# Performance work log

Measured on AMD Instinct MI355X. Metric: run time of the kernel, lower is better.

The kernel has to match this reference:

```python
import jax, jax.numpy as jnp
import numpy as np

ANGLE = 0.5  # angular margin from init_kwargs


def setup_inputs() -> dict:
    key = jax.random.key(0)
    k1, k2, k3 = jax.random.split(key, 3)
    B, F, C = 512, 128, 100000
    # scale by 0.1 so exp(features @ w) and exp(modulus * cos) stay finite in fp32
    features = jax.random.normal(k1, (B, F), dtype=jnp.float32) * 0.1
    w = jax.random.normal(k2, (F, C), dtype=jnp.float32) * 0.1
    target = jax.random.randint(k3, (B,), 0, C, dtype=jnp.int64)
    return {"features": features, "w": w, "target": target}


def reference(features, w, target):
    B = features.shape[0]
    rows = jnp.arange(B)
    # norms: [B,1] and [1,C]
    features_modulus = jnp.sqrt(jnp.sum(features ** 2, axis=1, keepdims=True))
    w_modulus = jnp.sqrt(jnp.sum(w ** 2, axis=0, keepdims=True))
    modulus = features_modulus * w_modulus  # [B, C]
    logits = jnp.matmul(features, w)  # [B, C] (computed once; torch computes it twice)
    cos_theta = logits / modulus / 1.01
    theta = jnp.arccos(cos_theta) + ANGLE
    cos_theta_plus = jnp.cos(theta)
    margin_logits = modulus * cos_theta_plus  # [B, C]
    top = jnp.exp(margin_logits[rows, target])  # [B]
    down_ = jnp.exp(logits)  # [B, C]
    down = jnp.sum(down_, axis=1) - down_[rows, target] + top  # [B]
    return -jnp.sum(jnp.log(top / down)) / B
```

## Files before the change

### kernel.cpp

```cpp
#include <hip/hip_runtime.h>

#define F_DIM 128
#define C_DIM 100000
#define B_ROWS 512
#define ANGLE 0.5f
#define CPB 128
#define NCB 782
#define OOB_PAD 96.0f

typedef __attribute__((ext_vector_type(4))) float  f32x4;
typedef __attribute__((ext_vector_type(8))) short  bf16x8;

static __device__ __forceinline__ short f2bf(float x) {
    unsigned int u = __float_as_uint(x);
    u += 0x7FFFu + ((u >> 16) & 1u);
    return (short)(u >> 16);
}

__global__ __launch_bounds__(512, 4)
void arc_main(const float* __restrict__ feat,
              const float* __restrict__ w,
              float* __restrict__ pp)
{
    __shared__ unsigned short lBt[128 * 128];

    const int tid = threadIdx.x;
    const int cb  = blockIdx.x;
    const int c0  = cb * CPB;
    const int r0  = blockIdx.y * 256;

    const int lane = tid & 63;
    const int wv   = tid >> 6;
    const int quad = lane >> 4;
    const int l15  = lane & 15;

    bf16x8 fB[2][4];
    #pragma unroll
    for (int s = 0; s < 2; ++s) {
        const int b = r0 + wv * 32 + s * 16 + l15;
        #pragma unroll
        for (int ks = 0; ks < 4; ++ks) {
            const int k0 = ks * 32 + quad * 8;
            const f32x4 u0 = *(const f32x4*)(feat + b * F_DIM + k0);
            const f32x4 u1 = *(const f32x4*)(feat + b * F_DIM + k0 + 4);
            bf16x8 h;
            h[0] = f2bf(u0[0]); h[1] = f2bf(u0[1]); h[2] = f2bf(u0[2]); h[3] = f2bf(u0[3]);
            h[4] = f2bf(u1[0]); h[5] = f2bf(u1[1]); h[6] = f2bf(u1[2]); h[7] = f2bf(u1[3]);
            fB[s][ks] = h;
        }
    }

    {
        const int c  = tid & 127;
        const int g  = tid >> 7;
        const int gc = c0 + c;
        #pragma unroll
        for (int j = 0; j < 4; ++j) {
            float v[8];
            #pragma unroll
            for (int i = 0; i < 8; ++i) {
                const int k = g * 32 + j * 8 + i;
                v[i] = (gc < C_DIM) ? w[(size_t)k * C_DIM + gc] : 0.f;
            }
            bf16x8 h;
            #pragma unroll
            for (int i = 0; i < 8; ++i) h[i] = f2bf(v[i]);
            const int pc = (g * 4 + j) ^ (c & 15);
            *(bf16x8*)&lBt[c * 128 + pc * 8] = h;
        }
    }
    __syncthreads();

    float eA0 = 0.f, eA1 = 0.f, eA2 = 0.f, eA3 = 0.f;
    float eB0 = 0.f, eB1 = 0.f, eB2 = 0.f, eB3 = 0.f;
    #pragma unroll
    for (int m = 0; m < 8; ++m) {
        f32x4 a0 = {0.f, 0.f, 0.f, 0.f};
        f32x4 a1 = {0.f, 0.f, 0.f, 0.f};
        const int row = m * 16 + l15;
        #pragma unroll
        for (int ks = 0; ks < 4; ++ks) {
            const int pc = (ks * 4 + quad) ^ (row & 15);
            const bf16x8 af = *(const bf16x8*)&lBt[row * 128 + pc * 8];
            a0 = __builtin_amdgcn_mfma_f32_16x16x32_bf16(af, fB[0][ks], a0, 0, 0, 0);
            a1 = __builtin_amdgcn_mfma_f32_16x16x32_bf16(af, fB[1][ks], a1, 0, 0, 0);
        }
        eA0 += __expf(a0[0]); eA1 += __expf(a0[1]);
        eA2 += __expf(a0[2]); eA3 += __expf(a0[3]);
        eB0 += __expf(a1[0]); eB1 += __expf(a1[1]);
        eB2 += __expf(a1[2]); eB3 += __expf(a1[3]);
    }

    float esum0 = (eA0 + eA1) + (eA2 + eA3);
    float esum1 = (eB0 + eB1) + (eB2 + eB3);
    esum0 += __shfl_xor(esum0, 16); esum0 += __shfl_xor(esum0, 32);
    esum1 += __shfl_xor(esum1, 16); esum1 += __shfl_xor(esum1, 32);
    if (lane < 16) {
        pp[(size_t)cb * 512 + r0 + wv * 32 + lane]      = esum0;
        pp[(size_t)cb * 512 + r0 + wv * 32 + 16 + lane] = esum1;
    }
}

__global__ void arc_row(const float* __restrict__ feat,
                        const float* __restrict__ w,
                        const int*   __restrict__ target,
                        const float* __restrict__ pp,
                        float* __restrict__ term)
{
    const int b    = blockIdx.x;
    const int lane = threadIdx.x;
    const int t    = target[b];

    float dot = 0.f, wsq = 0.f, fsq = 0.f, rs = 0.f;
    #pragma unroll
    for (int h = 0; h < 2; ++h) {
        const int f  = lane + h * 64;
        const float fv = feat[b * F_DIM + f];
        const float wv = w[(size_t)f * C_DIM + t];
        dot += fv * wv;
        wsq += wv * wv;
        fsq += fv * fv;
    }
    for (int j = lane; j < NCB; j += 64)
        rs += pp[(size_t)j * 512 + b];

    #pragma unroll
    for (int off = 32; off > 0; off >>= 1) {
        dot += __shfl_xor(dot, off);
        wsq += __shfl_xor(wsq, off);
        fsq += __shfl_xor(fsq, off);
        rs  += __shfl_xor(rs,  off);
    }
    if (lane == 0) {
        const float mod = sqrtf(fsq) * sqrtf(wsq);
        float ct = dot / (mod * 1.01f);
        ct = fminf(1.f, fmaxf(-1.f, ct));
        const float th   = acosf(ct) + ANGLE;
        const float marg = mod * cosf(th);
        const float down = rs - OOB_PAD - expf(dot) + expf(marg);
        term[b] = marg - logf(down);
    }
}

__global__ void arc_loss(const float* __restrict__ term,
                         float* __restrict__ out)
{
    __shared__ float red[B_ROWS];
    const int b = threadIdx.x;
    red[b] = term[b];
    __syncthreads();
    #pragma unroll
    for (int st = 256; st > 0; st >>= 1) {
        if (b < st) red[b] += red[b + st];
        __syncthreads();
    }
    if (b == 0) out[0] = -red[0] / (float)B_ROWS;
}

extern "C" void kernel_launch(void* const* d_in, const int* in_sizes, int n_in,
                              void* d_out, int out_size, void* d_ws, size_t ws_size,
                              hipStream_t stream)
{
    const float* feat   = (const float*)d_in[0];
    const float* w      = (const float*)d_in[1];
    const int*   target = (const int*)d_in[2];

    float* pp   = (float*)d_ws;
    float* term = pp + (size_t)NCB * 512;

    arc_main<<<dim3(NCB, 2), 512, 0, stream>>>(feat, w, pp);
    arc_row<<<B_ROWS, 64, 0, stream>>>(feat, w, target, pp, term);
    arc_loss<<<1, B_ROWS, 0, stream>>>(term, (float*)d_out);
}
```

Measured before the change: 131.5 us.

## Vectorize weight tile load, use hardware bf16 packing and exp2, transpose partials

The weight tile is now loaded as float4 vectors (four classes per thread across eight feature rows) instead of scalar loads, with a new LDS swizzle to match. fp32-to-bf16 conversion uses the packed hardware instruction instead of manual rounding. log2(e) is folded into the weights so the epilogue can use the native exp2. The partial-sum buffer is transposed to row-major so the row kernel reads contiguous memory. These target the global load and VALU cost of staging and the exp work, at the cost of a more intricate swizzle and scaling before the bf16 rounding.

Result: faster. 128.8 us (-2.1%).

```diff
diff --git a/kernel.cpp b/kernel.cpp
--- a/kernel.cpp
+++ b/kernel.cpp
@@ -1,20 +1,22 @@
 #include <hip/hip_runtime.h>
 
-#define F_DIM 128
-#define C_DIM 100000
-#define B_ROWS 512
-#define ANGLE 0.5f
-#define CPB 128
-#define NCB 782
+#define F_DIM   128
+#define C_DIM   100000
+#define B_ROWS  512
+#define ANGLE   0.5f
+#define CPB     128
+#define NCB     782
 #define OOB_PAD 96.0f
+#define LOG2E   1.4426950408889634f
 
-typedef __attribute__((ext_vector_type(4))) float  f32x4;
-typedef __attribute__((ext_vector_type(8))) short  bf16x8;
+typedef __attribute__((ext_vector_type(4))) float        f32x4;
+typedef __attribute__((ext_vector_type(8))) short        bf16x8;
+typedef __attribute__((ext_vector_type(4))) unsigned int u32x4;
 
-static __device__ __forceinline__ short f2bf(float x) {
-    unsigned int u = __float_as_uint(x);
-    u += 0x7FFFu + ((u >> 16) & 1u);
-    return (short)(u >> 16);
+static __device__ __forceinline__ unsigned int pk2(float a, float b) {
+    unsigned int r;
+    asm("v_cvt_pk_bf16_f32 %0, %1, %2" : "=v"(r) : "v"(a), "v"(b));
+    return r;
 }
 
 __global__ __launch_bounds__(512, 4)
@@ -24,15 +26,42 @@
 {
     __shared__ unsigned short lBt[128 * 128];
 
-    const int tid = threadIdx.x;
-    const int cb  = blockIdx.x;
-    const int c0  = cb * CPB;
-    const int r0  = blockIdx.y * 256;
-
+    const int tid  = threadIdx.x;
+    const int cb   = blockIdx.x;
+    const int c0   = cb * CPB;
+    const int r0   = blockIdx.y * 256;
     const int lane = tid & 63;
     const int wv   = tid >> 6;
     const int quad = lane >> 4;
     const int l15  = lane & 15;
+
+    {
+        const int cq = tid & 31;
+        const int ko = tid >> 5;
+        const int gc = c0 + cq * 4;
+        f32x4 wr[8];
+        if (gc < C_DIM) {
+            const float* wp = w + (size_t)ko * 8 * C_DIM + gc;
+            #pragma unroll
+            for (int i = 0; i < 8; ++i)
+                wr[i] = *(const f32x4*)(wp + (size_t)i * C_DIM);
+        } else {
+            #pragma unroll
+            for (int i = 0; i < 8; ++i)
+                wr[i] = (f32x4){0.f, 0.f, 0.f, 0.f};
+        }
+        #pragma unroll
+        for (int j = 0; j < 4; ++j) {
+            const int cls = cq * 4 + j;
+            union { u32x4 u; bf16x8 h; } c;
+            c.u[0] = pk2(wr[0][j] * LOG2E, wr[1][j] * LOG2E);
+            c.u[1] = pk2(wr[2][j] * LOG2E, wr[3][j] * LOG2E);
+            c.u[2] = pk2(wr[4][j] * LOG2E, wr[5][j] * LOG2E);
+            c.u[3] = pk2(wr[6][j] * LOG2E, wr[7][j] * LOG2E);
+            const int f = (cls & 12) | ((cls ^ (cls >> 4)) & 3);
+            *(bf16x8*)&lBt[cls * 128 + ((ko ^ f) << 3)] = c.h;
+        }
+    }
 
     bf16x8 fB[2][4];
     #pragma unroll
@@ -43,30 +72,10 @@
             const int k0 = ks * 32 + quad * 8;
             const f32x4 u0 = *(const f32x4*)(feat + b * F_DIM + k0);
             const f32x4 u1 = *(const f32x4*)(feat + b * F_DIM + k0 + 4);
-            bf16x8 h;
-            h[0] = f2bf(u0[0]); h[1] = f2bf(u0[1]); h[2] = f2bf(u0[2]); h[3] = f2bf(u0[3]);
-            h[4] = f2bf(u1[0]); h[5] = f2bf(u1[1]); h[6] = f2bf(u1[2]); h[7] = f2bf(u1[3]);
-            fB[s][ks] = h;
-        }
-    }
-
-    {
-        const int c  = tid & 127;
-        const int g  = tid >> 7;
-        const int gc = c0 + c;
-        #pragma unroll
-        for (int j = 0; j < 4; ++j) {
-            float v[8];
-            #pragma unroll
-            for (int i = 0; i < 8; ++i) {
-                const int k = g * 32 + j * 8 + i;
-                v[i] = (gc < C_DIM) ? w[(size_t)k * C_DIM + gc] : 0.f;
-            }
-            bf16x8 h;
-            #pragma unroll
-            for (int i = 0; i < 8; ++i) h[i] = f2bf(v[i]);
-            const int pc = (g * 4 + j) ^ (c & 15);
-            *(bf16x8*)&lBt[c * 128 + pc * 8] = h;
+            union { u32x4 u; bf16x8 h; } c;
+            c.u[0] = pk2(u0[0], u0[1]); c.u[1] = pk2(u0[2], u0[3]);
+            c.u[2] = pk2(u1[0], u1[1]); c.u[3] = pk2(u1[2], u1[3]);
+            fB[s][ks] = c.h;
         }
     }
     __syncthreads();
@@ -77,18 +86,19 @@
     for (int m = 0; m < 8; ++m) {
         f32x4 a0 = {0.f, 0.f, 0.f, 0.f};
         f32x4 a1 = {0.f, 0.f, 0.f, 0.f};
-        const int row = m * 16 + l15;
+        const int rb = (m * 16 + l15) * 128;
+        const int fr = (l15 & 12) | ((l15 ^ m) & 3);
         #pragma unroll
         for (int ks = 0; ks < 4; ++ks) {
-            const int pc = (ks * 4 + quad) ^ (row & 15);
-            const bf16x8 af = *(const bf16x8*)&lBt[row * 128 + pc * 8];
+            const int pc = (ks * 4 + quad) ^ fr;
+            const bf16x8 af = *(const bf16x8*)&lBt[rb + (pc << 3)];
             a0 = __builtin_amdgcn_mfma_f32_16x16x32_bf16(af, fB[0][ks], a0, 0, 0, 0);
             a1 = __builtin_amdgcn_mfma_f32_16x16x32_bf16(af, fB[1][ks], a1, 0, 0, 0);
         }
-        eA0 += __expf(a0[0]); eA1 += __expf(a0[1]);
-        eA2 += __expf(a0[2]); eA3 += __expf(a0[3]);
-        eB0 += __expf(a1[0]); eB1 += __expf(a1[1]);
-        eB2 += __expf(a1[2]); eB3 += __expf(a1[3]);
+        eA0 += __builtin_amdgcn_exp2f(a0[0]); eA1 += __builtin_amdgcn_exp2f(a0[1]);
+        eA2 += __builtin_amdgcn_exp2f(a0[2]); eA3 += __builtin_amdgcn_exp2f(a0[3]);
+        eB0 += __builtin_amdgcn_exp2f(a1[0]); eB1 += __builtin_amdgcn_exp2f(a1[1]);
+        eB2 += __builtin_amdgcn_exp2f(a1[2]); eB3 += __builtin_amdgcn_exp2f(a1[3]);
     }
 
     float esum0 = (eA0 + eA1) + (eA2 + eA3);
@@ -96,8 +106,9 @@
     esum0 += __shfl_xor(esum0, 16); esum0 += __shfl_xor(esum0, 32);
     esum1 += __shfl_xor(esum1, 16); esum1 += __shfl_xor(esum1, 32);
     if (lane < 16) {
-        pp[(size_t)cb * 512 + r0 + wv * 32 + lane]      = esum0;
-        pp[(size_t)cb * 512 + r0 + wv * 32 + 16 + lane] = esum1;
+        const int r = r0 + wv * 32 + lane;
+        pp[(size_t)r * NCB + cb]        = esum0;
+        pp[(size_t)(r + 16) * NCB + cb] = esum1;
     }
 }
 
@@ -114,15 +125,18 @@
     float dot = 0.f, wsq = 0.f, fsq = 0.f, rs = 0.f;
     #pragma unroll
     for (int h = 0; h < 2; ++h) {
-        const int f  = lane + h * 64;
+        const int f   = lane + h * 64;
         const float fv = feat[b * F_DIM + f];
-        const float wv = w[(size_t)f * C_DIM + t];
-        dot += fv * wv;
-        wsq += wv * wv;
+        const float wc = w[(size_t)f * C_DIM + t];
+        dot += fv * wc;
+        wsq += wc * wc;
         fsq += fv * fv;
     }
-    for (int j = lane; j < NCB; j += 64)
-        rs += pp[(size_t)j * 512 + b];
+    #pragma unroll
+    for (int j = 0; j < 13; ++j) {
+        const int c = lane + j * 64;
+        if (c < NCB) rs += pp[(size_t)b * NCB + c];
+    }
 
     #pragma unroll
     for (int off = 32; off > 0; off >>= 1) {
@@ -166,7 +180,7 @@
     const int*   target = (const int*)d_in[2];
 
     float* pp   = (float*)d_ws;
-    float* term = pp + (size_t)NCB * 512;
+    float* term = pp + (size_t)B_ROWS * NCB;
 
     arc_main<<<dim3(NCB, 2), 512, 0, stream>>>(feat, w, pp);
     arc_row<<<B_ROWS, 64, 0, stream>>>(feat, w, target, pp, term);
```
